# Performance work log

Measured on AMD Instinct MI355X. Metric: run time of the kernel, lower is better.

## Reference

```python
import jax, jax.numpy as jnp
import numpy as np

N = 100_000
E = 1_600_000
IN, HID, OUT = 128, 128, 64
TAU = 0.67


def setup_inputs() -> dict:
    key = jax.random.key(0)
    ks = jax.random.split(key, 8)
    x = jax.random.normal(ks[0], (N, IN), dtype=jnp.float32)
    edge_index = jax.random.randint(ks[1], (2, E), 0, N, dtype=jnp.int32)
    spi = jnp.float32(0.8)
    def lin(k, fi, fo):
        return jax.random.normal(k, (fi, fo), dtype=jnp.float32) / np.sqrt(fi)
    return {
        "x": x,
        "edge_index": edge_index,
        "spi": spi,
        "Wg1": lin(ks[2], IN, HID), "bg1": jnp.zeros((HID,), jnp.float32),
        "Wg2": lin(ks[3], HID, OUT), "bg2": jnp.zeros((OUT,), jnp.float32),
        "Wm1": lin(ks[4], IN, HID), "bm1": jnp.zeros((HID,), jnp.float32),
        "Wm2": lin(ks[5], HID, OUT), "bm2": jnp.zeros((OUT,), jnp.float32),
        "log_T": jnp.float32(np.log(0.1)),
    }


def _gcn_layer(h, W, b, src, dst, norm, n):
    # h: [N, Fin] -> linear, gather along src, scale by sym-norm, scatter-add to dst
    h = h @ W                                   # [N, Fout]
    msg = h[src] * norm[:, None]                # [E+N, Fout]
    agg = jax.ops.segment_sum(msg, dst, num_segments=n)
    return agg + b


def reference(x, edge_index, spi, Wg1, bg1, Wg2, bg2, Wm1, bm1, Wm2, bm2, log_T):
    n = x.shape[0]
    loop = jnp.arange(n, dtype=edge_index.dtype)
    src = jnp.concatenate([edge_index[0], loop])
    dst = jnp.concatenate([edge_index[1], loop])
    # symmetric normalization with self-loops (PyG GCNConv default)
    deg = jax.ops.segment_sum(jnp.ones(src.shape[0], x.dtype), dst, num_segments=n)
    dis = jax.lax.rsqrt(deg)                    # deg >= 1 due to self-loops
    norm = dis[src] * dis[dst]                  # [E+N]

    # GNN branch (dropout inactive in eval mode)
    z = jax.nn.relu(_gcn_layer(x, Wg1, bg1, src, dst, norm, n))
    z_gnn = _gcn_layer(z, Wg2, bg2, src, dst, norm, n)

    # MLP branch
    z_mlp = jax.nn.relu(x @ Wm1 + bm1) @ Wm2 + bm2

    # SPI-guided gating
    beta = jax.nn.sigmoid((spi - TAU) / jnp.exp(log_T))
    z_fused = beta * z_gnn + (1.0 - beta) * z_mlp
    return z_fused
```

## Files before the change

kernel.cpp:

```cpp
#include <hip/hip_runtime.h>
#include <math.h>

__global__ void rank_kernel(const int* __restrict__ ei, int* __restrict__ cnt,
                            int* __restrict__ rank, int E) {
  int e = blockIdx.x * 256 + threadIdx.x;
  if (e < E) rank[e] = atomicAdd(&cnt[ei[E + e]], 1);
}

__global__ void scan_block_kernel(const int* __restrict__ cnt, int* __restrict__ part,
                                  int* __restrict__ bsums, float* __restrict__ dis, int n) {
  __shared__ int wsum[4];
  int tid = threadIdx.x;
  int lane = tid & 63, wid = tid >> 6;
  int base = blockIdx.x * 1024 + tid * 4;
  int v0 = 0, v1 = 0, v2 = 0, v3 = 0;
  if (base + 0 < n) { v0 = cnt[base + 0]; dis[base + 0] = 1.f / sqrtf((float)(v0 + 1)); }
  if (base + 1 < n) { v1 = cnt[base + 1]; dis[base + 1] = 1.f / sqrtf((float)(v1 + 1)); }
  if (base + 2 < n) { v2 = cnt[base + 2]; dis[base + 2] = 1.f / sqrtf((float)(v2 + 1)); }
  if (base + 3 < n) { v3 = cnt[base + 3]; dis[base + 3] = 1.f / sqrtf((float)(v3 + 1)); }
  int tot = v0 + v1 + v2 + v3;
  int x = tot;
#pragma unroll
  for (int d = 1; d < 64; d <<= 1) { int y = __shfl_up(x, d, 64); if (lane >= d) x += y; }
  if (lane == 63) wsum[wid] = x;
  __syncthreads();
  int wpre = 0;
#pragma unroll
  for (int w = 0; w < 4; ++w) wpre += (w < wid) ? wsum[w] : 0;
  int ex = wpre + x - tot;
  if (base + 0 < n) part[base + 0] = ex; ex += v0;
  if (base + 1 < n) part[base + 1] = ex; ex += v1;
  if (base + 2 < n) part[base + 2] = ex; ex += v2;
  if (base + 3 < n) part[base + 3] = ex;
  if (tid == 255) bsums[blockIdx.x] = wpre + x;
}

__global__ void scan_tops_kernel(int* __restrict__ bsums, int nb, int* __restrict__ offs, int n) {
  int lane = threadIdx.x;
  int run = 0;
  for (int base = 0; base < nb; base += 64) {
    int i = base + lane;
    int v = (i < nb) ? bsums[i] : 0;
    int x = v;
#pragma unroll
    for (int d = 1; d < 64; d <<= 1) { int y = __shfl_up(x, d, 64); if (lane >= d) x += y; }
    if (i < nb) bsums[i] = run + x - v;
    run += __shfl(x, 63, 64);
  }
  if (lane == 0) offs[n] = run;
}

__global__ void scan_add_kernel(const int* __restrict__ bsums, int* __restrict__ offs, int n) {
  int i = blockIdx.x * 256 + threadIdx.x;
  if (i < n) offs[i] += bsums[i >> 10];
}

__global__ void scatter_kernel(const int* __restrict__ ei, const int* __restrict__ rank,
                               const int* __restrict__ offs, int* __restrict__ csr, int E) {
  int e = blockIdx.x * 256 + threadIdx.x;
  if (e < E) {
    int s = ei[e];
    int d = ei[E + e];
    csr[offs[d] + rank[e]] = s;
  }
}


template <int NCOL, bool RELU, bool BIAS>
__global__ __launch_bounds__(256) void gemm_kernel(const float* __restrict__ A,
                                                   const float* __restrict__ W,
                                                   const float* __restrict__ bias,
                                                   float* __restrict__ C, int M) {
  constexpr int TN = NCOL / 16;
  __shared__ float Wt[NCOL * 128];
  int tid = threadIdx.x;
  int row0 = blockIdx.x * 128;

  constexpr int WI = (128 * (NCOL / 4)) / 256;
#pragma unroll
  for (int i = 0; i < WI; ++i) {
    int idx = tid + i * 256;
    int k = idx / (NCOL / 4);
    int c0 = (idx % (NCOL / 4)) * 4;
    float4 v = *reinterpret_cast<const float4*>(W + k * NCOL + c0);
    int k4 = k >> 2, kk = k & 3;
    Wt[(c0 + 0) * 128 + ((k4 ^ (((c0 + 0) >> 3) & 7)) << 2) + kk] = v.x;
    Wt[(c0 + 1) * 128 + ((k4 ^ (((c0 + 1) >> 3) & 7)) << 2) + kk] = v.y;
    Wt[(c0 + 2) * 128 + ((k4 ^ (((c0 + 2) >> 3) & 7)) << 2) + kk] = v.z;
    Wt[(c0 + 3) * 128 + ((k4 ^ (((c0 + 3) >> 3) & 7)) << 2) + kk] = v.w;
  }

  int tx = tid & 15, ty = tid >> 4;
  int cbase = tx * TN;
  int sw = (cbase >> 3) & 7;

  const float* Ar[8];
#pragma unroll
  for (int r = 0; r < 8; ++r) {
    int gr = row0 + ty * 8 + r;
    if (gr > M - 1) gr = M - 1;
    Ar[r] = A + (size_t)gr * 128;
  }

  float acc[8][TN];
#pragma unroll
  for (int r = 0; r < 8; ++r)
#pragma unroll
    for (int c = 0; c < TN; ++c) acc[r][c] = 0.f;

  float4 a0[8], a1[8];
#pragma unroll
  for (int r = 0; r < 8; ++r) a0[r] = *reinterpret_cast<const float4*>(Ar[r] + 0);

  __syncthreads();

#pragma unroll 1
  for (int k4 = 0; k4 < 32; k4 += 2) {
#pragma unroll
    for (int r = 0; r < 8; ++r)
      a1[r] = *reinterpret_cast<const float4*>(Ar[r] + (k4 + 1) * 4);
    {
      int wo = (k4 ^ sw) << 2;
#pragma unroll
      for (int c = 0; c < TN; ++c) {
        float4 w = *reinterpret_cast<const float4*>(&Wt[(cbase + c) * 128 + wo]);
#pragma unroll
        for (int r = 0; r < 8; ++r) {
          acc[r][c] = fmaf(a0[r].x, w.x, acc[r][c]);
          acc[r][c] = fmaf(a0[r].y, w.y, acc[r][c]);
          acc[r][c] = fmaf(a0[r].z, w.z, acc[r][c]);
          acc[r][c] = fmaf(a0[r].w, w.w, acc[r][c]);
        }
      }
    }
    int kn = k4 + 2 < 31 ? k4 + 2 : 31;
#pragma unroll
    for (int r = 0; r < 8; ++r)
      a0[r] = *reinterpret_cast<const float4*>(Ar[r] + kn * 4);
    {
      int wo = ((k4 + 1) ^ sw) << 2;
#pragma unroll
      for (int c = 0; c < TN; ++c) {
        float4 w = *reinterpret_cast<const float4*>(&Wt[(cbase + c) * 128 + wo]);
#pragma unroll
        for (int r = 0; r < 8; ++r) {
          acc[r][c] = fmaf(a1[r].x, w.x, acc[r][c]);
          acc[r][c] = fmaf(a1[r].y, w.y, acc[r][c]);
          acc[r][c] = fmaf(a1[r].z, w.z, acc[r][c]);
          acc[r][c] = fmaf(a1[r].w, w.w, acc[r][c]);
        }
      }
    }
  }

#pragma unroll
  for (int r = 0; r < 8; ++r) {
    int gr = row0 + ty * 8 + r;
    if (gr < M) {
#pragma unroll
      for (int c = 0; c < TN; c += 4) {
        float4 o;
        float v0 = acc[r][c + 0], v1 = acc[r][c + 1], v2 = acc[r][c + 2], v3 = acc[r][c + 3];
        if (BIAS) {
          v0 += bias[cbase + c + 0]; v1 += bias[cbase + c + 1];
          v2 += bias[cbase + c + 2]; v3 += bias[cbase + c + 3];
        }
        if (RELU) {
          v0 = fmaxf(v0, 0.f); v1 = fmaxf(v1, 0.f);
          v2 = fmaxf(v2, 0.f); v3 = fmaxf(v3, 0.f);
        }
        o.x = v0; o.y = v1; o.z = v2; o.w = v3;
        *reinterpret_cast<float4*>(C + (size_t)gr * NCOL + cbase + c) = o;
      }
    }
  }
}


__global__ __launch_bounds__(256) void agg1_kernel(const float* __restrict__ h,
                                                   const int* __restrict__ offs,
                                                   const int* __restrict__ csr,
                                                   const float* __restrict__ dis,
                                                   const float* __restrict__ b,
                                                   float* __restrict__ zout, int n) {
  int wid = threadIdx.x >> 6, lane = threadIdx.x & 63;
  int node = blockIdx.x * 4 + wid;
  if (node >= n) return;
  int half = lane >> 5;
  int fl = (lane & 31) << 2;
  float dn = dis[node];
  float4 acc = make_float4(0.f, 0.f, 0.f, 0.f);
  if (half == 0) {
    float4 hv = *reinterpret_cast<const float4*>(h + (size_t)node * 128 + fl);
    float s2 = dn * dn;
    acc.x = hv.x * s2; acc.y = hv.y * s2; acc.z = hv.z * s2; acc.w = hv.w * s2;
  }
  int jb = offs[node], je = offs[node + 1];
  for (int bs = jb; bs < je; bs += 64) {
    int idx = bs + lane;
    int sl = 0; float wl = 0.f;
    if (idx < je) { sl = csr[idx]; wl = dis[sl] * dn; }
    int m = je - bs; if (m > 64) m = 64;
    for (int t = 0; t < m; t += 4) {
      int e0 = t + half, e1 = t + 2 + half;
      int s0 = __shfl(sl, e0, 64); float w0 = __shfl(wl, e0, 64);
      int s1 = __shfl(sl, e1, 64); float w1 = __shfl(wl, e1, 64);
      float4 v0 = *reinterpret_cast<const float4*>(h + (size_t)s0 * 128 + fl);
      float4 v1 = *reinterpret_cast<const float4*>(h + (size_t)s1 * 128 + fl);
      acc.x = fmaf(v0.x, w0, acc.x); acc.y = fmaf(v0.y, w0, acc.y);
      acc.z = fmaf(v0.z, w0, acc.z); acc.w = fmaf(v0.w, w0, acc.w);
      acc.x = fmaf(v1.x, w1, acc.x); acc.y = fmaf(v1.y, w1, acc.y);
      acc.z = fmaf(v1.z, w1, acc.z); acc.w = fmaf(v1.w, w1, acc.w);
    }
  }
  acc.x += __shfl_xor(acc.x, 32, 64);
  acc.y += __shfl_xor(acc.y, 32, 64);
  acc.z += __shfl_xor(acc.z, 32, 64);
  acc.w += __shfl_xor(acc.w, 32, 64);
  if (lane < 32) {
    float4 bb = *reinterpret_cast<const float4*>(b + fl);
    float4 o;
    o.x = fmaxf(acc.x + bb.x, 0.f);
    o.y = fmaxf(acc.y + bb.y, 0.f);
    o.z = fmaxf(acc.z + bb.z, 0.f);
    o.w = fmaxf(acc.w + bb.w, 0.f);
    *reinterpret_cast<float4*>(zout + (size_t)node * 128 + fl) = o;
  }
}

__global__ __launch_bounds__(256) void agg2_kernel(const float* __restrict__ h,
                                                   const int* __restrict__ offs,
                                                   const int* __restrict__ csr,
                                                   const float* __restrict__ dis,
                                                   const float* __restrict__ b,
                                                   const float* __restrict__ zmlp,
                                                   const float* __restrict__ spi,
                                                   const float* __restrict__ logT,
                                                   float* __restrict__ out, int n) {
  int wid = threadIdx.x >> 6, lane = threadIdx.x & 63;
  int node = blockIdx.x * 4 + wid;
  if (node >= n) return;
  int slot = lane >> 4;
  int fl = (lane & 15) << 2;
  float dn = dis[node];
  float4 acc = make_float4(0.f, 0.f, 0.f, 0.f);
  if (slot == 0) {
    float4 hv = *reinterpret_cast<const float4*>(h + (size_t)node * 64 + fl);
    float s2 = dn * dn;
    acc.x = hv.x * s2; acc.y = hv.y * s2; acc.z = hv.z * s2; acc.w = hv.w * s2;
  }
  int jb = offs[node], je = offs[node + 1];
  for (int bs = jb; bs < je; bs += 64) {
    int idx = bs + lane;
    int sl = 0; float wl = 0.f;
    if (idx < je) { sl = csr[idx]; wl = dis[sl] * dn; }
    int m = je - bs; if (m > 64) m = 64;
    for (int t = 0; t < m; t += 8) {
      int e0 = t + slot, e1 = t + 4 + slot;
      int s0 = __shfl(sl, e0, 64); float w0 = __shfl(wl, e0, 64);
      int s1 = __shfl(sl, e1, 64); float w1 = __shfl(wl, e1, 64);
      float4 v0 = *reinterpret_cast<const float4*>(h + (size_t)s0 * 64 + fl);
      float4 v1 = *reinterpret_cast<const float4*>(h + (size_t)s1 * 64 + fl);
      acc.x = fmaf(v0.x, w0, acc.x); acc.y = fmaf(v0.y, w0, acc.y);
      acc.z = fmaf(v0.z, w0, acc.z); acc.w = fmaf(v0.w, w0, acc.w);
      acc.x = fmaf(v1.x, w1, acc.x); acc.y = fmaf(v1.y, w1, acc.y);
      acc.z = fmaf(v1.z, w1, acc.z); acc.w = fmaf(v1.w, w1, acc.w);
    }
  }
  acc.x += __shfl_xor(acc.x, 16, 64);
  acc.y += __shfl_xor(acc.y, 16, 64);
  acc.z += __shfl_xor(acc.z, 16, 64);
  acc.w += __shfl_xor(acc.w, 16, 64);
  acc.x += __shfl_xor(acc.x, 32, 64);
  acc.y += __shfl_xor(acc.y, 32, 64);
  acc.z += __shfl_xor(acc.z, 32, 64);
  acc.w += __shfl_xor(acc.w, 32, 64);
  if (lane < 16) {
    float beta = 1.f / (1.f + expf(-((spi[0] - 0.67f) / expf(logT[0]))));
    float4 bb = *reinterpret_cast<const float4*>(b + fl);
    float4 mv = *reinterpret_cast<const float4*>(zmlp + (size_t)node * 64 + fl);
    float4 o;
    o.x = beta * (acc.x + bb.x) + (1.f - beta) * mv.x;
    o.y = beta * (acc.y + bb.y) + (1.f - beta) * mv.y;
    o.z = beta * (acc.z + bb.z) + (1.f - beta) * mv.z;
    o.w = beta * (acc.w + bb.w) + (1.f - beta) * mv.w;
    *reinterpret_cast<float4*>(out + (size_t)node * 64 + fl) = o;
  }
}


extern "C" void kernel_launch(void* const* d_in, const int* in_sizes, int n_in,
                              void* d_out, int out_size, void* d_ws, size_t ws_size,
                              hipStream_t stream) {
  const float* x    = (const float*)d_in[0];
  const int*   ei   = (const int*)d_in[1];
  const float* spi  = (const float*)d_in[2];
  const float* Wg1  = (const float*)d_in[3];
  const float* bg1  = (const float*)d_in[4];
  const float* Wg2  = (const float*)d_in[5];
  const float* bg2  = (const float*)d_in[6];
  const float* Wm1  = (const float*)d_in[7];
  const float* bm1  = (const float*)d_in[8];
  const float* Wm2  = (const float*)d_in[9];
  const float* bm2  = (const float*)d_in[10];
  const float* logT = (const float*)d_in[11];
  float* out = (float*)d_out;

  int n = in_sizes[0] / 128;
  int E = in_sizes[1] / 2;
  int nb = (n + 1023) / 1024;

  char* p = (char*)d_ws;
  auto alloc = [&](size_t bytes) -> char* {
    char* r = p;
    p += (bytes + 255) & ~(size_t)255;
    return r;
  };
  int*   cnt    = (int*)alloc((size_t)n * 4);
  int*   offs   = (int*)alloc((size_t)(n + 1) * 4);
  float* dis    = (float*)alloc((size_t)n * 4);
  int*   bsums  = (int*)alloc((size_t)nb * 4);
  int*   rank   = (int*)alloc((size_t)E * 4);
  int*   csr    = (int*)alloc((size_t)E * 4);
  float* h1     = (float*)alloc((size_t)n * 128 * 4);
  float* hm     = (float*)alloc((size_t)n * 128 * 4);
  float* z      = (float*)alloc((size_t)n * 128 * 4);

  hipMemsetAsync(cnt, 0, (size_t)n * 4, stream);

  int eb = (E + 255) / 256;
  rank_kernel<<<eb, 256, 0, stream>>>(ei, cnt, rank, E);
  scan_block_kernel<<<nb, 256, 0, stream>>>(cnt, offs, bsums, dis, n);
  scan_tops_kernel<<<1, 64, 0, stream>>>(bsums, nb, offs, n);
  scan_add_kernel<<<(n + 255) / 256, 256, 0, stream>>>(bsums, offs, n);
  scatter_kernel<<<eb, 256, 0, stream>>>(ei, rank, offs, csr, E);

  int gb = (n + 127) / 128;
  gemm_kernel<128, false, false><<<gb, 256, 0, stream>>>(x, Wg1, nullptr, h1, n);
  gemm_kernel<128, true,  true ><<<gb, 256, 0, stream>>>(x, Wm1, bm1, hm, n);
  agg1_kernel<<<(n + 3) / 4, 256, 0, stream>>>(h1, offs, csr, dis, bg1, z, n);

  float* h2   = h1;
  gemm_kernel<64, false, false><<<gb, 256, 0, stream>>>(z, Wg2, nullptr, h2, n);
  float* zmlp = z;
  gemm_kernel<64, false, true ><<<gb, 256, 0, stream>>>(hm, Wm2, bm2, zmlp, n);

  agg2_kernel<<<(n + 3) / 4, 256, 0, stream>>>(h2, offs, csr, dis, bg2, zmlp, spi, logT, out, n);
}
```

Measured before the change: 607.8 us.

## Merge rank counting with first-layer GEMMs and pair second-layer GEMMs per launch

Folds the edge rank/atomic-count pass into the same launch as the two first-layer GEMMs, splitting the grid between GEMM tiles and edge blocks so the memory-bound atomics overlap with compute. The two second-layer GEMMs are likewise merged into one launch with interleaved blocks. The aggregation loops are unrolled to four gathers per iteration with two accumulators to raise memory-level parallelism. The rank buffer is reused as zmlp storage to save workspace, which assumes rank is dead before the second GEMM launch. The fused first kernel's large shared allocation applies to the atomic blocks too and may limit occupancy for them.

```diff
diff --git a/kernel.cpp b/kernel.cpp
--- a/kernel.cpp
+++ b/kernel.cpp
@@ -1,11 +1,6 @@
 #include <hip/hip_runtime.h>
 #include <math.h>
 
-__global__ void rank_kernel(const int* __restrict__ ei, int* __restrict__ cnt,
-                            int* __restrict__ rank, int E) {
-  int e = blockIdx.x * 256 + threadIdx.x;
-  if (e < E) rank[e] = atomicAdd(&cnt[ei[E + e]], 1);
-}
 
 __global__ void scan_block_kernel(const int* __restrict__ cnt, int* __restrict__ part,
                                   int* __restrict__ bsums, float* __restrict__ dis, int n) {
@@ -67,14 +62,12 @@
 
 
 template <int NCOL, bool RELU, bool BIAS>
-__global__ __launch_bounds__(256) void gemm_kernel(const float* __restrict__ A,
-                                                   const float* __restrict__ W,
-                                                   const float* __restrict__ bias,
-                                                   float* __restrict__ C, int M) {
+__device__ void gemm_tile(const float* __restrict__ A, const float* __restrict__ W,
+                          const float* __restrict__ bias, float* __restrict__ C,
+                          int M, int block, float* Wt) {
   constexpr int TN = NCOL / 16;
-  __shared__ float Wt[NCOL * 128];
   int tid = threadIdx.x;
-  int row0 = blockIdx.x * 128;
+  int row0 = block * 128;
 
   constexpr int WI = (128 * (NCOL / 4)) / 256;
 #pragma unroll
@@ -177,6 +170,42 @@
 }
 
 
+__global__ __launch_bounds__(256) void k1_fused(const int* __restrict__ ei, int* __restrict__ cnt,
+                                                int* __restrict__ rank, int E,
+                                                const float* __restrict__ x,
+                                                const float* __restrict__ Wg1, float* __restrict__ h1,
+                                                const float* __restrict__ Wm1,
+                                                const float* __restrict__ bm1, float* __restrict__ hm,
+                                                int M, int nG) {
+  __shared__ float Wt[128 * 128];
+  int b = blockIdx.x;
+  int NB = gridDim.x;
+  int g0 = (int)(((long)b * nG) / NB);
+  int g1 = (int)(((long)(b + 1) * nG) / NB);
+  if (g1 > g0) {
+    if (g0 < nG / 2) gemm_tile<128, false, false>(x, Wg1, nullptr, h1, M, g0, Wt);
+    else             gemm_tile<128, true,  true >(x, Wm1, bm1,    hm, M, g0 - nG / 2, Wt);
+  } else {
+    int r = b - g0;
+    int e = r * 256 + threadIdx.x;
+    if (e < E) rank[e] = atomicAdd(&cnt[ei[E + e]], 1);
+  }
+}
+
+
+__global__ __launch_bounds__(256) void k8_fused(const float* __restrict__ z,
+                                                const float* __restrict__ Wg2, float* __restrict__ h2,
+                                                const float* __restrict__ hm,
+                                                const float* __restrict__ Wm2,
+                                                const float* __restrict__ bm2, float* __restrict__ zmlp,
+                                                int M) {
+  __shared__ float Wt[64 * 128];
+  int b = blockIdx.x;
+  if ((b & 1) == 0) gemm_tile<64, false, false>(z,  Wg2, nullptr, h2,   M, b >> 1, Wt);
+  else              gemm_tile<64, false, true >(hm, Wm2, bm2,    zmlp, M, b >> 1, Wt);
+}
+
+
 __global__ __launch_bounds__(256) void agg1_kernel(const float* __restrict__ h,
                                                    const int* __restrict__ offs,
                                                    const int* __restrict__ csr,
@@ -190,6 +219,7 @@
   int fl = (lane & 31) << 2;
   float dn = dis[node];
   float4 acc = make_float4(0.f, 0.f, 0.f, 0.f);
+  float4 acc2 = make_float4(0.f, 0.f, 0.f, 0.f);
   if (half == 0) {
     float4 hv = *reinterpret_cast<const float4*>(h + (size_t)node * 128 + fl);
     float s2 = dn * dn;
@@ -201,18 +231,26 @@
     int sl = 0; float wl = 0.f;
     if (idx < je) { sl = csr[idx]; wl = dis[sl] * dn; }
     int m = je - bs; if (m > 64) m = 64;
-    for (int t = 0; t < m; t += 4) {
-      int e0 = t + half, e1 = t + 2 + half;
-      int s0 = __shfl(sl, e0, 64); float w0 = __shfl(wl, e0, 64);
-      int s1 = __shfl(sl, e1, 64); float w1 = __shfl(wl, e1, 64);
+    for (int t = 0; t < m; t += 8) {
+      int s0 = __shfl(sl, t + half,     64); float w0 = __shfl(wl, t + half,     64);
+      int s1 = __shfl(sl, t + 2 + half, 64); float w1 = __shfl(wl, t + 2 + half, 64);
+      int s2 = __shfl(sl, t + 4 + half, 64); float w2 = __shfl(wl, t + 4 + half, 64);
+      int s3 = __shfl(sl, t + 6 + half, 64); float w3 = __shfl(wl, t + 6 + half, 64);
       float4 v0 = *reinterpret_cast<const float4*>(h + (size_t)s0 * 128 + fl);
       float4 v1 = *reinterpret_cast<const float4*>(h + (size_t)s1 * 128 + fl);
-      acc.x = fmaf(v0.x, w0, acc.x); acc.y = fmaf(v0.y, w0, acc.y);
-      acc.z = fmaf(v0.z, w0, acc.z); acc.w = fmaf(v0.w, w0, acc.w);
-      acc.x = fmaf(v1.x, w1, acc.x); acc.y = fmaf(v1.y, w1, acc.y);
-      acc.z = fmaf(v1.z, w1, acc.z); acc.w = fmaf(v1.w, w1, acc.w);
-    }
-  }
+      float4 v2 = *reinterpret_cast<const float4*>(h + (size_t)s2 * 128 + fl);
+      float4 v3 = *reinterpret_cast<const float4*>(h + (size_t)s3 * 128 + fl);
+      acc.x  = fmaf(v0.x, w0, acc.x);  acc.y  = fmaf(v0.y, w0, acc.y);
+      acc.z  = fmaf(v0.z, w0, acc.z);  acc.w  = fmaf(v0.w, w0, acc.w);
+      acc.x  = fmaf(v1.x, w1, acc.x);  acc.y  = fmaf(v1.y, w1, acc.y);
+      acc.z  = fmaf(v1.z, w1, acc.z);  acc.w  = fmaf(v1.w, w1, acc.w);
+      acc2.x = fmaf(v2.x, w2, acc2.x); acc2.y = fmaf(v2.y, w2, acc2.y);
+      acc2.z = fmaf(v2.z, w2, acc2.z); acc2.w = fmaf(v2.w, w2, acc2.w);
+      acc2.x = fmaf(v3.x, w3, acc2.x); acc2.y = fmaf(v3.y, w3, acc2.y);
+      acc2.z = fmaf(v3.z, w3, acc2.z); acc2.w = fmaf(v3.w, w3, acc2.w);
+    }
+  }
+  acc.x += acc2.x; acc.y += acc2.y; acc.z += acc2.z; acc.w += acc2.w;
   acc.x += __shfl_xor(acc.x, 32, 64);
   acc.y += __shfl_xor(acc.y, 32, 64);
   acc.z += __shfl_xor(acc.z, 32, 64);
@@ -244,6 +282,7 @@
   int fl = (lane & 15) << 2;
   float dn = dis[node];
   float4 acc = make_float4(0.f, 0.f, 0.f, 0.f);
+  float4 acc2 = make_float4(0.f, 0.f, 0.f, 0.f);
   if (slot == 0) {
     float4 hv = *reinterpret_cast<const float4*>(h + (size_t)node * 64 + fl);
     float s2 = dn * dn;
@@ -255,18 +294,26 @@
     int sl = 0; float wl = 0.f;
     if (idx < je) { sl = csr[idx]; wl = dis[sl] * dn; }
     int m = je - bs; if (m > 64) m = 64;
-    for (int t = 0; t < m; t += 8) {
-      int e0 = t + slot, e1 = t + 4 + slot;
-      int s0 = __shfl(sl, e0, 64); float w0 = __shfl(wl, e0, 64);
-      int s1 = __shfl(sl, e1, 64); float w1 = __shfl(wl, e1, 64);
+    for (int t = 0; t < m; t += 16) {
+      int s0 = __shfl(sl, t + slot,      64); float w0 = __shfl(wl, t + slot,      64);
+      int s1 = __shfl(sl, t + 4 + slot,  64); float w1 = __shfl(wl, t + 4 + slot,  64);
+      int s2 = __shfl(sl, t + 8 + slot,  64); float w2 = __shfl(wl, t + 8 + slot,  64);
+      int s3 = __shfl(sl, t + 12 + slot, 64); float w3 = __shfl(wl, t + 12 + slot, 64);
       float4 v0 = *reinterpret_cast<const float4*>(h + (size_t)s0 * 64 + fl);
       float4 v1 = *reinterpret_cast<const float4*>(h + (size_t)s1 * 64 + fl);
-      acc.x = fmaf(v0.x, w0, acc.x); acc.y = fmaf(v0.y, w0, acc.y);
-      acc.z = fmaf(v0.z, w0, acc.z); acc.w = fmaf(v0.w, w0, acc.w);
-      acc.x = fmaf(v1.x, w1, acc.x); acc.y = fmaf(v1.y, w1, acc.y);
-      acc.z = fmaf(v1.z, w1, acc.z); acc.w = fmaf(v1.w, w1, acc.w);
-    }
-  }
+      float4 v2 = *reinterpret_cast<const float4*>(h + (size_t)s2 * 64 + fl);
+      float4 v3 = *reinterpret_cast<const float4*>(h + (size_t)s3 * 64 + fl);
+      acc.x  = fmaf(v0.x, w0, acc.x);  acc.y  = fmaf(v0.y, w0, acc.y);
+      acc.z  = fmaf(v0.z, w0, acc.z);  acc.w  = fmaf(v0.w, w0, acc.w);
+      acc.x  = fmaf(v1.x, w1, acc.x);  acc.y  = fmaf(v1.y, w1, acc.y);
+      acc.z  = fmaf(v1.z, w1, acc.z);  acc.w  = fmaf(v1.w, w1, acc.w);
+      acc2.x = fmaf(v2.x, w2, acc2.x); acc2.y = fmaf(v2.y, w2, acc2.y);
+      acc2.z = fmaf(v2.z, w2, acc2.z); acc2.w = fmaf(v2.w, w2, acc2.w);
+      acc2.x = fmaf(v3.x, w3, acc2.x); acc2.y = fmaf(v3.y, w3, acc2.y);
+      acc2.z = fmaf(v3.z, w3, acc2.z); acc2.w = fmaf(v3.w, w3, acc2.w);
+    }
+  }
+  acc.x += acc2.x; acc.y += acc2.y; acc.z += acc2.z; acc.w += acc2.w;
   acc.x += __shfl_xor(acc.x, 16, 64);
   acc.y += __shfl_xor(acc.y, 16, 64);
   acc.z += __shfl_xor(acc.z, 16, 64);
@@ -320,7 +367,9 @@
   int*   offs   = (int*)alloc((size_t)(n + 1) * 4);
   float* dis    = (float*)alloc((size_t)n * 4);
   int*   bsums  = (int*)alloc((size_t)nb * 4);
-  int*   rank   = (int*)alloc((size_t)E * 4);
+  char*  ru     = alloc((size_t)n * 64 * 4);
+  int*   rank   = (int*)ru;
+  float* zmlp   = (float*)ru;
   int*   csr    = (int*)alloc((size_t)E * 4);
   float* h1     = (float*)alloc((size_t)n * 128 * 4);
   float* hm     = (float*)alloc((size_t)n * 128 * 4);
@@ -329,21 +378,20 @@
   hipMemsetAsync(cnt, 0, (size_t)n * 4, stream);
 
   int eb = (E + 255) / 256;
-  rank_kernel<<<eb, 256, 0, stream>>>(ei, cnt, rank, E);
+  int gb = (n + 127) / 128;
+  int nG = 2 * gb;
+
+  k1_fused<<<eb + nG, 256, 0, stream>>>(ei, cnt, rank, E, x, Wg1, h1, Wm1, bm1, hm, n, nG);
+
   scan_block_kernel<<<nb, 256, 0, stream>>>(cnt, offs, bsums, dis, n);
   scan_tops_kernel<<<1, 64, 0, stream>>>(bsums, nb, offs, n);
   scan_add_kernel<<<(n + 255) / 256, 256, 0, stream>>>(bsums, offs, n);
   scatter_kernel<<<eb, 256, 0, stream>>>(ei, rank, offs, csr, E);
 
-  int gb = (n + 127) / 128;
-  gemm_kernel<128, false, false><<<gb, 256, 0, stream>>>(x, Wg1, nullptr, h1, n);
-  gemm_kernel<128, true,  true ><<<gb, 256, 0, stream>>>(x, Wm1, bm1, hm, n);
   agg1_kernel<<<(n + 3) / 4, 256, 0, stream>>>(h1, offs, csr, dis, bg1, z, n);
 
-  float* h2   = h1;
-  gemm_kernel<64, false, false><<<gb, 256, 0, stream>>>(z, Wg2, nullptr, h2, n);
-  float* zmlp = z;
-  gemm_kernel<64, false, true ><<<gb, 256, 0, stream>>>(hm, Wm2, bm2, zmlp, n);
+  float* h2 = h1;
+  k8_fused<<<2 * gb, 256, 0, stream>>>(z, Wg2, h2, hm, Wm2, bm2, zmlp, n);
 
   agg2_kernel<<<(n + 3) / 4, 256, 0, stream>>>(h2, offs, csr, dis, bg2, zmlp, spi, logT, out, n);
 }
```

New measurement: 587.3 us. 1.04x faster.
